# Kernel optimization log

Hardware: AMD Instinct MI355X
Metric: run time of the kernel (lower is better)

Reference implementation:

```python
import jax, jax.numpy as jnp
import numpy as np

EPS = 1e-6
AREA_WIDTH = 3
NHEAD = 8
DIM = 16


def _skew(v):
    # v: [N,3] -> [N,3,3] cross-product matrix
    x, y, z = v[..., 0], v[..., 1], v[..., 2]
    zero = jnp.zeros_like(x)
    return jnp.stack([
        jnp.stack([zero, -z, y], -1),
        jnp.stack([z, zero, -x], -1),
        jnp.stack([-y, x, zero], -1)], -2)


def _create_meshgrid(h, w):
    # kornia create_meshgrid(..., normalized=False): last dim is (x, y), row-major flatten
    xs = jnp.arange(w, dtype=jnp.float32)
    ys = jnp.arange(h, dtype=jnp.float32)
    gx, gy = jnp.meshgrid(xs, ys, indexing='xy')  # [h,w]
    return jnp.stack([gx, gy], -1).reshape(h * w, 2)  # [S,2]


def _epipolar_lines(coord, R, t, K0, K1):
    # coord [S,2]; R [N,3,3]; t [N,3,1] -> lines [N,S,3] (unit-normalized a,b), mode [N,S]
    S = coord.shape[0]
    p = jnp.concatenate([coord, jnp.ones((S, 1), coord.dtype)], -1)  # [S,3]
    E = _skew(t[..., 0]) @ R                                         # [t]_x R
    F = jnp.swapaxes(jnp.linalg.inv(K1), -1, -2) @ E @ jnp.linalg.inv(K0)
    lines = jnp.einsum('nij,sj->nsi', F, p)
    n = jnp.linalg.norm(lines[..., :2], axis=-1, keepdims=True)
    lines = lines / jnp.maximum(n, 1e-12)
    mode = jnp.abs(lines[..., 1]) >= jnp.abs(lines[..., 0])  # True: solve y(x) (|b|>=|a|)
    return lines, mode


def _get_mask(lines, mode, coord, area_width):
    # lines [N,L,3], mode [N,L], coord [S,2] -> within [N,L,S]
    a, b, c = lines[..., 0], lines[..., 1], lines[..., 2]
    xs, ys = coord[:, 0], coord[:, 1]
    hw = area_width / 2.0
    safe = lambda d: jnp.where(jnp.abs(d) < 1e-12, 1e-12, d)
    cy = (-a / safe(b))[..., None] * xs + (-c / safe(b))[..., None]  # [N,L,S]
    cx = (-b / safe(a))[..., None] * ys + (-c / safe(a))[..., None]
    wy = (ys < cy + hw) & (ys > cy - hw)
    wx = (xs < cx + hw) & (xs > cx - hw)
    return jnp.where(mode[..., None], wy, wx)


def _gather_index(within, C):
    # sort-based top-C compaction, index 0 doubles as padding (faithful to source)
    S = within.shape[-1]
    idx = jnp.arange(S, dtype=jnp.int32)
    ti = jnp.where(within, idx[None, None, :], 0)
    ti = jnp.sort(ti, axis=-1)[..., -C:]
    return ti, ti != 0


def _feature_map(x):
    return jax.nn.elu(x) + 1.0


def reference(queries, keys, values, solved_sample, K0, K1, R, t, h0c, w0c, scale):
    N, L, H, D = queries.shape
    sol = np.asarray(solved_sample).astype(bool)  # static split of the batch
    sol_idx = np.nonzero(sol)[0]
    uns_idx = np.nonzero(~sol)[0]
    Q = _feature_map(queries)
    K = _feature_map(keys)
    out = jnp.zeros((N, L, H, D), queries.dtype)

    if sol_idx.size > 0:  # epipolar-gathered candidate attention, direction '0to1'
        coord = _create_meshgrid(h0c, w0c)
        K0s = K0[sol_idx].at[:, :2, :].mul(1.0 / scale)
        K1s = K1[sol_idx].at[:, :2, :].mul(1.0 / scale)
        C = max(h0c, w0c) * AREA_WIDTH
        lines, mode = _epipolar_lines(coord, R[sol_idx], t[sol_idx], K0s, K1s)
        within = _get_mask(lines, mode, coord, AREA_WIDTH)       # [Ns,L,S]
        index, mask = _gather_index(within, C)                    # [Ns,L,C]
        Ns = sol_idx.size
        n_ix = jnp.arange(Ns)[:, None, None]
        Qs = Q[sol_idx]
        Ks = K[sol_idx][n_ix, index]            # [Ns,L,C,H,D]
        Vs = values[sol_idx][n_ix, index]
        m = mask[..., None, None].astype(Ks.dtype)
        Ks = Ks * m
        Vs = Vs * m / C
        KV = jnp.einsum('nlchd,nlchv->nlhdv', Ks, Vs)
        Z = 1.0 / (jnp.einsum('nlhd,nlhd->nlh', Qs, Ks.sum(2)) + EPS)
        out = out.at[sol_idx].set(jnp.einsum('nlhd,nlhdv,nlh->nlhv', Qs, KV, Z) * C)

    if uns_idx.size > 0:  # plain linear attention
        Qu, Ku, Vu = Q[uns_idx], K[uns_idx], values[uns_idx]
        S = Ku.shape[1]
        KV = jnp.einsum('nshd,nshv->nhdv', Ku, Vu / S)
        Z = 1.0 / (jnp.einsum('nlhd,nhd->nlh', Qu, Ku.sum(1)) + EPS)
        out = out.at[uns_idx].set(jnp.einsum('nlhd,nhdv,nlh->nlhv', Qu, KV, Z) * S)
    return out


def setup_inputs() -> dict:
    key = jax.random.key(0)
    kq, kk, kv = jax.random.split(key, 3)
    N, H, D = 4, NHEAD, DIM
    h0c, w0c = 48, 64
    L = h0c * w0c
    queries = jax.random.normal(kq, (N, L, H, D), jnp.float32)
    keys = jax.random.normal(kk, (N, L, H, D), jnp.float32)
    values = jax.random.normal(kv, (N, L, H, D), jnp.float32)
    solved_sample = jnp.array([True, True, False, False])
    Kmat = np.array([[600., 0., 256.], [0., 600., 192.], [0., 0., 1.]], np.float32)
    K0 = jnp.asarray(np.tile(Kmat, (N, 1, 1)))
    Rl, tl = [], []
    for i in range(N):
        th = 0.05 * (i + 1)
        Rl.append(np.array([[np.cos(th), 0., np.sin(th)], [0., 1., 0.],
                            [-np.sin(th), 0., np.cos(th)]], np.float32))
        tl.append(np.array([[0.2 + 0.01 * i], [0.05], [0.02]], np.float32))
    R = jnp.asarray(np.stack(Rl))
    t = jnp.asarray(np.stack(tl))
    return {"queries": queries, "keys": keys, "values": values,
            "solved_sample": solved_sample, "K0": K0, "K1": K0, "R": R, "t": t,
            "h0c": h0c, "w0c": w0c, "scale": 8}
```

## Files before the change

### kernel.cpp

```cpp
#include <hip/hip_runtime.h>
#include <math.h>

#define NHEAD 8
#define DIM   16
#define EPSF  1e-6f
#define KVCH  8

typedef _Float16 half2_t __attribute__((ext_vector_type(2)));
typedef _Float16 half4_t __attribute__((ext_vector_type(4)));
typedef _Float16 half8_t __attribute__((ext_vector_type(8)));

#if defined(__has_builtin)
#if __has_builtin(__builtin_amdgcn_fdot2)
#define HAVE_FDOT2 1
#endif
#endif

__device__ __forceinline__ float dot2(half2_t a, half2_t b, float c) {
#ifdef HAVE_FDOT2
    return __builtin_amdgcn_fdot2(a, b, c, false);
#else
    return c + (float)a.x * (float)b.x + (float)a.y * (float)b.y;
#endif
}

__device__ __forceinline__ bool solved_flag(const void* p, int i) {
    const unsigned int* u = (const unsigned int*)p;
    unsigned int v0 = u[0];
    if (v0 <= 1u)             return u[i] != 0u;
    if (v0 == 0x3F800000u)    return ((const float*)p)[i] != 0.0f;
    return ((const unsigned char*)p)[i] != 0;
}

__device__ __forceinline__ float fm(float x) {
    return x > 0.f ? x + 1.f : expf(x);
}

__device__ void inv3d(const double* M, double* inv) {
    double det = M[0]*(M[4]*M[8]-M[5]*M[7]) - M[1]*(M[3]*M[8]-M[5]*M[6]) + M[2]*(M[3]*M[7]-M[4]*M[6]);
    double id = 1.0 / det;
    inv[0] =  (M[4]*M[8]-M[5]*M[7])*id;
    inv[1] = -(M[1]*M[8]-M[2]*M[7])*id;
    inv[2] =  (M[1]*M[5]-M[2]*M[4])*id;
    inv[3] = -(M[3]*M[8]-M[5]*M[6])*id;
    inv[4] =  (M[0]*M[8]-M[2]*M[6])*id;
    inv[5] = -(M[0]*M[5]-M[2]*M[3])*id;
    inv[6] =  (M[3]*M[7]-M[4]*M[6])*id;
    inv[7] = -(M[0]*M[7]-M[1]*M[6])*id;
    inv[8] =  (M[0]*M[4]-M[1]*M[3])*id;
}

__device__ void compute_F_one(const float* K0, const float* K1, const float* R,
                              const float* t, float invs, float* Fout, int n) {
    double A[9], B[9];
    for (int i = 0; i < 9; ++i) {
        float a = K0[n*9 + i], b = K1[n*9 + i];
        if (i < 6) { a *= invs; b *= invs; }
        A[i] = (double)a; B[i] = (double)b;
    }
    double iA[9], iB[9];
    inv3d(A, iA); inv3d(B, iB);
    double tx = t[n*3+0], ty = t[n*3+1], tz = t[n*3+2];
    double S[9] = {0.0,-tz,ty, tz,0.0,-tx, -ty,tx,0.0};
    double E[9], M[9];
    for (int i = 0; i < 3; ++i)
        for (int j = 0; j < 3; ++j) {
            double s = 0.0;
            for (int k = 0; k < 3; ++k) s += S[i*3+k] * (double)R[n*9 + k*3 + j];
            E[i*3+j] = s;
        }
    for (int i = 0; i < 3; ++i)
        for (int j = 0; j < 3; ++j) {
            double s = 0.0;
            for (int k = 0; k < 3; ++k) s += E[i*3+k] * iA[k*3+j];
            M[i*3+j] = s;
        }
    for (int i = 0; i < 3; ++i)
        for (int j = 0; j < 3; ++j) {
            double s = 0.0;
            for (int k = 0; k < 3; ++k) s += iB[k*3+i] * M[k*3+j];
            Fout[n*9 + i*3 + j] = (float)s;
        }
}

__launch_bounds__(256)
__global__ void prep_kv(const float4* __restrict__ Kr4, const float4* __restrict__ Vr4,
                        _Float16* __restrict__ Kh, _Float16* __restrict__ Vh, int n4,
                        const float* __restrict__ Kr, const float* __restrict__ Vr,
                        const void* __restrict__ flags,
                        float* __restrict__ KVp, float* __restrict__ Ksp,
                        const float* __restrict__ K0, const float* __restrict__ K1,
                        const float* __restrict__ R,  const float* __restrict__ t,
                        const int* __restrict__ scale_p, float* __restrict__ Fout,
                        int N, int L, int PB) {
    if ((int)blockIdx.x < PB) {
        int i = blockIdx.x * 256 + threadIdx.x;
        if (i < n4) {
            float4 k = Kr4[i];
            half4_t kh = { (_Float16)fm(k.x), (_Float16)fm(k.y), (_Float16)fm(k.z), (_Float16)fm(k.w) };
            ((half4_t*)Kh)[i] = kh;
            float4 v = Vr4[i];
            half4_t vh = { (_Float16)v.x, (_Float16)v.y, (_Float16)v.z, (_Float16)v.w };
            ((half4_t*)Vh)[i] = vh;
        }
        if (blockIdx.x == 0) {
            if (threadIdx.x < (unsigned)N) {
                float invs = 1.0f / (float)(*scale_p);
                compute_F_one(K0, K1, R, t, invs, Fout, threadIdx.x);
            }
            if (threadIdx.x >= 64 && threadIdx.x < 192) {
                int tz = threadIdx.x - 64;
                size_t zr = (size_t)N * L * 128 + tz;
                Kh[zr] = (_Float16)0.f;
                Vh[zr] = (_Float16)0.f;
            }
        }
    } else {
        int kb = blockIdx.x - PB;
        int chunk = kb & (KVCH - 1);
        int h = (kb >> 3) & 7;
        int n = kb >> 6;
        if (n >= N || solved_flag(flags, n)) return;
        int tdx = threadIdx.x;
        int d = tdx >> 4, v = tdx & 15;
        int rowsPer = (L + KVCH - 1) / KVCH;
        int r0 = chunk * rowsPer;
        int r1 = min(r0 + rowsPer, L);
        const float* Kb = Kr + (size_t)n * L * (NHEAD * DIM) + h * DIM;
        const float* Vb = Vr + (size_t)n * L * (NHEAD * DIM) + h * DIM;
        float acc = 0.f, ks = 0.f;
        #pragma unroll 8
        for (int s = r0; s < r1; ++s) {
            float kd = fm(Kb[(size_t)s * (NHEAD * DIM) + d]);
            float vv = Vb[(size_t)s * (NHEAD * DIM) + v];
            acc += kd * vv;
            ks  += kd;
        }
        KVp[(((size_t)chunk * N + n) * NHEAD + h) * 256 + (d << 4) + v] = acc;
        if (v == 0) Ksp[(((size_t)chunk * N + n) * NHEAD + h) * 16 + d] = ks;
    }
}

__launch_bounds__(256)
__global__ void mega(const float* __restrict__ Qr,
                     const _Float16* __restrict__ Kh, const _Float16* __restrict__ Vh,
                     const void* __restrict__ flags,  const float* __restrict__ F,
                     const float* __restrict__ KVp,   const float* __restrict__ Ksp,
                     float* __restrict__ outp,
                     const int* __restrict__ h0c_p, const int* __restrict__ w0c_p,
                     int N, int L, int Bs) {
    __shared__ int    tbl[4][96];
    __shared__ float2 comb[2][64];
    __shared__ float  dcomb[2][8];
    if ((int)blockIdx.x < Bs) {
        int w    = threadIdx.x >> 6;
        int p    = w & 1;
        int qp   = w >> 1;
        int lane = threadIdx.x & 63;
        int q    = blockIdx.x * 2 + qp;
        int n    = q / L;
        if (n >= N) return;
        if (!solved_flag(flags, n)) return;
        int NL = N * L;
        int s = q - n * L;
        int W  = *w0c_p;
        int Hc = *h0c_p;
        float px = (float)(s % W);
        float py = (float)(s / W);

        const float* Fn = F + n * 9;
        float a = Fn[0]*px + Fn[1]*py + Fn[2];
        float b = Fn[3]*px + Fn[4]*py + Fn[5];
        float c = Fn[6]*px + Fn[7]*py + Fn[8];
        float nrm = sqrtf(a*a + b*b);
        float mdiv = fmaxf(nrm, 1e-12f);
        a /= mdiv; b /= mdiv; c /= mdiv;
        bool mode = fabsf(b) >= fabsf(a);

        float slope, inter;
        int outerN, innerMax, sI, sO;
        if (mode) {
            float bs = (fabsf(b) < 1e-12f) ? 1e-12f : b;
            slope = -a / bs; inter = -c / bs;
            outerN = W; innerMax = Hc; sI = W; sO = 1;
        } else {
            float as = (fabsf(a) < 1e-12f) ? 1e-12f : a;
            slope = -b / as; inter = -c / as;
            outerN = Hc; innerMax = W; sI = 1; sO = W;
        }

        int c8 = lane >> 3;
        int h  = lane & 7;
        int h16 = h << 4;

        const float4* q4 = (const float4*)(Qr + (size_t)q * (NHEAD * DIM) + h16);
        half2_t q2[8];
        {
            float4 a0 = q4[0], a1 = q4[1], a2 = q4[2], a3 = q4[3];
            q2[0] = (half2_t){ (_Float16)fm(a0.x), (_Float16)fm(a0.y) };
            q2[1] = (half2_t){ (_Float16)fm(a0.z), (_Float16)fm(a0.w) };
            q2[2] = (half2_t){ (_Float16)fm(a1.x), (_Float16)fm(a1.y) };
            q2[3] = (half2_t){ (_Float16)fm(a1.z), (_Float16)fm(a1.w) };
            q2[4] = (half2_t){ (_Float16)fm(a2.x), (_Float16)fm(a2.y) };
            q2[5] = (half2_t){ (_Float16)fm(a2.z), (_Float16)fm(a2.w) };
            q2[6] = (half2_t){ (_Float16)fm(a3.x), (_Float16)fm(a3.y) };
            q2[7] = (half2_t){ (_Float16)fm(a3.z), (_Float16)fm(a3.w) };
        }

        int totalC = outerN * 3;
        int zsent  = NL << 7;
        const float hw = 1.5f;
        for (int tt = lane; tt < 96; tt += 64) {
            int g = tt >> 3, c8t = tt & 7;
            int m = (g << 4) | (p << 3) | c8t;
            int o = (int)((unsigned)m / 3u);
            int j = m - o * 3;
            float cc = fmaf(slope, (float)o, inter);
            float lo = cc - hw, hi = cc + hw;
            int ii = (int)floorf(lo) + 1 + j;
            float fi = (float)ii;
            bool valid = (m < totalC) && (ii >= 0) && (ii < innerMax)
                         && (fi > lo) && (fi < hi);
            int s2 = ii * sI + o * sO;
            valid = valid && (s2 != 0);
            tbl[w][tt] = valid ? ((n * L + s2) << 7) : zsent;
        }
        __syncthreads();

        half2_t acc2[8];
        #pragma unroll
        for (int i = 0; i < 8; ++i) acc2[i] = (half2_t){ (_Float16)0.f, (_Float16)0.f };
        float den = 0.f;

        int groups = (totalC + 15) >> 4;
        #pragma unroll 3
        for (int g = 0; g < groups; ++g) {
            int entry = tbl[w][(g << 3) + c8];
            const half8_t* kr = (const half8_t*)(Kh + entry + h16);
            const half8_t* vr = (const half8_t*)(Vh + entry + h16);
            half8_t k0 = kr[0], k1 = kr[1];
            half8_t v0 = vr[0], v1 = vr[1];
            union H8 { half8_t v; half2_t h[4]; };
            H8 ku0, ku1, vu0, vu1;
            ku0.v = k0; ku1.v = k1; vu0.v = v0; vu1.v = v1;
            float sA = 0.f, sB = 0.f;
            sA = dot2(q2[0], ku0.h[0], sA);
            sB = dot2(q2[1], ku0.h[1], sB);
            sA = dot2(q2[2], ku0.h[2], sA);
            sB = dot2(q2[3], ku0.h[3], sB);
            sA = dot2(q2[4], ku1.h[0], sA);
            sB = dot2(q2[5], ku1.h[1], sB);
            sA = dot2(q2[6], ku1.h[2], sA);
            sB = dot2(q2[7], ku1.h[3], sB);
            float sc = sA + sB;
            den += sc;
            _Float16 sch = (_Float16)sc;
            half2_t scv = (half2_t){ sch, sch };
            acc2[0] += scv * vu0.h[0];
            acc2[1] += scv * vu0.h[1];
            acc2[2] += scv * vu0.h[2];
            acc2[3] += scv * vu0.h[3];
            acc2[4] += scv * vu1.h[0];
            acc2[5] += scv * vu1.h[1];
            acc2[6] += scv * vu1.h[2];
            acc2[7] += scv * vu1.h[3];
        }

        den += __shfl_xor(den, 8);
        den += __shfl_xor(den, 16);
        den += __shfl_xor(den, 32);

        bool hi8 = (lane & 8) != 0;
        half2_t t4[4];
        #pragma unroll
        for (int j2 = 0; j2 < 4; ++j2) {
            half2_t send = hi8 ? acc2[j2] : acc2[4 + j2];
            int rr = __shfl_xor(__builtin_bit_cast(int, send), 8);
            half2_t keep = hi8 ? acc2[4 + j2] : acc2[j2];
            t4[j2] = keep + __builtin_bit_cast(half2_t, rr);
        }
        bool hi16 = (lane & 16) != 0;
        half2_t t2[2];
        #pragma unroll
        for (int j2 = 0; j2 < 2; ++j2) {
            half2_t send = hi16 ? t4[j2] : t4[2 + j2];
            int rr = __shfl_xor(__builtin_bit_cast(int, send), 16);
            half2_t keep = hi16 ? t4[2 + j2] : t4[j2];
            t2[j2] = keep + __builtin_bit_cast(half2_t, rr);
        }
        bool hi32 = (lane & 32) != 0;
        half2_t t1;
        {
            half2_t send = hi32 ? t2[0] : t2[1];
            int rr = __shfl_xor(__builtin_bit_cast(int, send), 32);
            half2_t keep = hi32 ? t2[1] : t2[0];
            t1 = keep + __builtin_bit_cast(half2_t, rr);
        }
        int e0 = (hi8 ? 8 : 0) + (hi16 ? 4 : 0) + (hi32 ? 2 : 0);

        if (p == 1) {
            comb[qp][lane] = make_float2((float)t1.x, (float)t1.y);
            if (lane < 8) dcomb[qp][lane] = den;
        }
        __syncthreads();
        if (p == 0) {
            float2 oth = comb[qp][lane];
            float dtot = den + dcomb[qp][h];
            float r = 1.0f / (dtot + EPSF);
            float2 o2 = { ((float)t1.x + oth.x) * r, ((float)t1.y + oth.y) * r };
            *(float2*)(outp + (size_t)q * (NHEAD * DIM) + h16 + e0) = o2;
        }
    } else {
        long long tot2 = (long long)N * L * NHEAD * DIM / 2;
        long long idx2 = (long long)(blockIdx.x - Bs) * 256 + threadIdx.x;
        if (idx2 >= tot2) return;
        int pp = (int)(idx2 & 63);
        int h = pp >> 3;
        int v = (pp & 7) * 2;
        long long ns = idx2 >> 6;
        int n = (int)(ns / L);
        if (solved_flag(flags, n)) return;
        const float* qrow = Qr + ns * (NHEAD * DIM) + h * DIM;
        float num0 = 0.f, num1 = 0.f, den = 0.f;
        #pragma unroll
        for (int d = 0; d < 16; ++d) {
            float qd = fm(qrow[d]);
            #pragma unroll
            for (int cch = 0; cch < KVCH; ++cch) {
                const float2 kv2 = *(const float2*)(KVp + (((size_t)cch * N + n) * NHEAD + h) * 256 + (d << 4) + v);
                num0 += qd * kv2.x;
                num1 += qd * kv2.y;
                den  += qd * Ksp[(((size_t)cch * N + n) * NHEAD + h) * 16 + d];
            }
        }
        float rdiv = 1.0f / (den + EPSF);
        size_t ob = ns * (NHEAD * DIM) + h * DIM + v;
        outp[ob]     = num0 * rdiv;
        outp[ob + 1] = num1 * rdiv;
    }
}

extern "C" void kernel_launch(void* const* d_in, const int* in_sizes, int n_in,
                              void* d_out, int out_size, void* d_ws, size_t ws_size,
                              hipStream_t stream) {
    const float* Qr   = (const float*)d_in[0];
    const float* Kr   = (const float*)d_in[1];
    const float* Vr   = (const float*)d_in[2];
    const void*  flag = d_in[3];
    const float* K0   = (const float*)d_in[4];
    const float* K1   = (const float*)d_in[5];
    const float* R    = (const float*)d_in[6];
    const float* t    = (const float*)d_in[7];
    const int*   h0c  = (const int*)d_in[8];
    const int*   w0c  = (const int*)d_in[9];
    const int*   scl  = (const int*)d_in[10];

    int N = in_sizes[3];
    int T = in_sizes[0];
    int L = T / (N * NHEAD * DIM);

    size_t arr = (size_t)T + 8 * 128;
    _Float16* Kh = (_Float16*)d_ws;
    _Float16* Vh = Kh + arr;
    float* Fm   = (float*)(Vh + arr);
    float* KVp  = Fm + (size_t)N * 9;
    float* Ksp  = KVp + (size_t)KVCH * N * NHEAD * 256;

    float* outp = (float*)d_out;

    int n4 = T / 4;
    int PB = (n4 + 255) / 256;
    int KB = N * NHEAD * KVCH;
    prep_kv<<<PB + KB, 256, 0, stream>>>((const float4*)Kr, (const float4*)Vr,
                                         Kh, Vh, n4, Kr, Vr, flag, KVp, Ksp,
                                         K0, K1, R, t, scl, Fm, N, L, PB);

    int Bs = (N * L) / 2;
    long long tot2 = (long long)N * L * NHEAD * DIM / 2;
    int Bu = (int)((tot2 + 255) / 256);
    mega<<<Bs + Bu, 256, 0, stream>>>(Qr, Kh, Vh, flag, Fm, KVp, Ksp, outp,
                                      h0c, w0c, N, L, Bs);
}
```

Baseline: 178.5 us.

## Process one query per wavefront with split-head lane mapping

Each wavefront now handles one full query instead of two wavefronts splitting a query's candidates. Lanes pair up to cover the 16-dim heads in halves, and dot products are combined with a lane-1 shuffle. This removes the cross-wavefront shared-memory combine and its second barrier, and halves the number of blocks. The cost is more shuffle reductions over all accumulators, plus an output store done by only 16 lanes. The index-table offsets are rescaled to byte offsets.

```diff
diff --git a/kernel.cpp b/kernel.cpp
--- a/kernel.cpp
+++ b/kernel.cpp
@@ -149,15 +149,11 @@
                      float* __restrict__ outp,
                      const int* __restrict__ h0c_p, const int* __restrict__ w0c_p,
                      int N, int L, int Bs) {
-    __shared__ int    tbl[4][96];
-    __shared__ float2 comb[2][64];
-    __shared__ float  dcomb[2][8];
+    __shared__ int tbl[4][192];
     if ((int)blockIdx.x < Bs) {
         int w    = threadIdx.x >> 6;
-        int p    = w & 1;
-        int qp   = w >> 1;
         int lane = threadIdx.x & 63;
-        int q    = blockIdx.x * 2 + qp;
+        int q    = blockIdx.x * 4 + w;
         int n    = q / L;
         if (n >= N) return;
         if (!solved_flag(flags, n)) return;
@@ -191,28 +187,26 @@
 
         int c8 = lane >> 3;
         int h  = lane & 7;
-        int h16 = h << 4;
-
-        const float4* q4 = (const float4*)(Qr + (size_t)q * (NHEAD * DIM) + h16);
-        half2_t q2[8];
+
+        const float4* qb = (const float4*)(Qr + (size_t)q * (NHEAD * DIM));
+        half2_t ql[4], qh[4];
         {
-            float4 a0 = q4[0], a1 = q4[1], a2 = q4[2], a3 = q4[3];
-            q2[0] = (half2_t){ (_Float16)fm(a0.x), (_Float16)fm(a0.y) };
-            q2[1] = (half2_t){ (_Float16)fm(a0.z), (_Float16)fm(a0.w) };
-            q2[2] = (half2_t){ (_Float16)fm(a1.x), (_Float16)fm(a1.y) };
-            q2[3] = (half2_t){ (_Float16)fm(a1.z), (_Float16)fm(a1.w) };
-            q2[4] = (half2_t){ (_Float16)fm(a2.x), (_Float16)fm(a2.y) };
-            q2[5] = (half2_t){ (_Float16)fm(a2.z), (_Float16)fm(a2.w) };
-            q2[6] = (half2_t){ (_Float16)fm(a3.x), (_Float16)fm(a3.y) };
-            q2[7] = (half2_t){ (_Float16)fm(a3.z), (_Float16)fm(a3.w) };
+            float4 a0 = qb[2*h], a1 = qb[2*h + 1];
+            float4 b0 = qb[16 + 2*h], b1 = qb[16 + 2*h + 1];
+            ql[0] = (half2_t){ (_Float16)fm(a0.x), (_Float16)fm(a0.y) };
+            ql[1] = (half2_t){ (_Float16)fm(a0.z), (_Float16)fm(a0.w) };
+            ql[2] = (half2_t){ (_Float16)fm(a1.x), (_Float16)fm(a1.y) };
+            ql[3] = (half2_t){ (_Float16)fm(a1.z), (_Float16)fm(a1.w) };
+            qh[0] = (half2_t){ (_Float16)fm(b0.x), (_Float16)fm(b0.y) };
+            qh[1] = (half2_t){ (_Float16)fm(b0.z), (_Float16)fm(b0.w) };
+            qh[2] = (half2_t){ (_Float16)fm(b1.x), (_Float16)fm(b1.y) };
+            qh[3] = (half2_t){ (_Float16)fm(b1.z), (_Float16)fm(b1.w) };
         }
 
         int totalC = outerN * 3;
-        int zsent  = NL << 7;
+        int zsent  = NL << 8;
         const float hw = 1.5f;
-        for (int tt = lane; tt < 96; tt += 64) {
-            int g = tt >> 3, c8t = tt & 7;
-            int m = (g << 4) | (p << 3) | c8t;
+        for (int m = lane; m < 192; m += 64) {
             int o = (int)((unsigned)m / 3u);
             int j = m - o * 3;
             float cc = fmaf(slope, (float)o, inter);
@@ -223,92 +217,81 @@
                          && (fi > lo) && (fi < hi);
             int s2 = ii * sI + o * sO;
             valid = valid && (s2 != 0);
-            tbl[w][tt] = valid ? ((n * L + s2) << 7) : zsent;
+            tbl[w][m] = valid ? ((n * L + s2) << 8) : zsent;
         }
         __syncthreads();
 
-        half2_t acc2[8];
+        half2_t accl[4], acch[4];
         #pragma unroll
-        for (int i = 0; i < 8; ++i) acc2[i] = (half2_t){ (_Float16)0.f, (_Float16)0.f };
-        float den = 0.f;
-
-        int groups = (totalC + 15) >> 4;
+        for (int i = 0; i < 4; ++i) {
+            accl[i] = (half2_t){ (_Float16)0.f, (_Float16)0.f };
+            acch[i] = (half2_t){ (_Float16)0.f, (_Float16)0.f };
+        }
+        float denl = 0.f, denh = 0.f;
+
+        int groups = (totalC + 7) >> 3;
+        int hoff = h << 4;
         #pragma unroll 3
         for (int g = 0; g < groups; ++g) {
-            int entry = tbl[w][(g << 3) + c8];
-            const half8_t* kr = (const half8_t*)(Kh + entry + h16);
-            const half8_t* vr = (const half8_t*)(Vh + entry + h16);
-            half8_t k0 = kr[0], k1 = kr[1];
-            half8_t v0 = vr[0], v1 = vr[1];
+            int off = tbl[w][(g << 3) + c8];
+            const char* kp = (const char*)Kh + off + hoff;
+            const char* vp = (const char*)Vh + off + hoff;
+            half8_t klo = *(const half8_t*)kp;
+            half8_t khi = *(const half8_t*)(kp + 128);
+            half8_t vlo = *(const half8_t*)vp;
+            half8_t vhi = *(const half8_t*)(vp + 128);
             union H8 { half8_t v; half2_t h[4]; };
-            H8 ku0, ku1, vu0, vu1;
-            ku0.v = k0; ku1.v = k1; vu0.v = v0; vu1.v = v1;
-            float sA = 0.f, sB = 0.f;
-            sA = dot2(q2[0], ku0.h[0], sA);
-            sB = dot2(q2[1], ku0.h[1], sB);
-            sA = dot2(q2[2], ku0.h[2], sA);
-            sB = dot2(q2[3], ku0.h[3], sB);
-            sA = dot2(q2[4], ku1.h[0], sA);
-            sB = dot2(q2[5], ku1.h[1], sB);
-            sA = dot2(q2[6], ku1.h[2], sA);
-            sB = dot2(q2[7], ku1.h[3], sB);
-            float sc = sA + sB;
-            den += sc;
-            _Float16 sch = (_Float16)sc;
-            half2_t scv = (half2_t){ sch, sch };
-            acc2[0] += scv * vu0.h[0];
-            acc2[1] += scv * vu0.h[1];
-            acc2[2] += scv * vu0.h[2];
-            acc2[3] += scv * vu0.h[3];
-            acc2[4] += scv * vu1.h[0];
-            acc2[5] += scv * vu1.h[1];
-            acc2[6] += scv * vu1.h[2];
-            acc2[7] += scv * vu1.h[3];
-        }
-
-        den += __shfl_xor(den, 8);
-        den += __shfl_xor(den, 16);
-        den += __shfl_xor(den, 32);
-
-        bool hi8 = (lane & 8) != 0;
-        half2_t t4[4];
+            H8 kl, kh2, vl, vh2;
+            kl.v = klo; kh2.v = khi; vl.v = vlo; vh2.v = vhi;
+            float pl = 0.f, ph = 0.f;
+            pl = dot2(ql[0], kl.h[0], pl);
+            ph = dot2(qh[0], kh2.h[0], ph);
+            pl = dot2(ql[1], kl.h[1], pl);
+            ph = dot2(qh[1], kh2.h[1], ph);
+            pl = dot2(ql[2], kl.h[2], pl);
+            ph = dot2(qh[2], kh2.h[2], ph);
+            pl = dot2(ql[3], kl.h[3], pl);
+            ph = dot2(qh[3], kh2.h[3], ph);
+            float sl = pl + __shfl_xor(pl, 1);
+            float sh = ph + __shfl_xor(ph, 1);
+            denl += sl;
+            denh += sh;
+            _Float16 slh = (_Float16)sl, shh = (_Float16)sh;
+            half2_t slv = (half2_t){ slh, slh };
+            half2_t shv = (half2_t){ shh, shh };
+            accl[0] += slv * vl.h[0];  acch[0] += shv * vh2.h[0];
+            accl[1] += slv * vl.h[1];  acch[1] += shv * vh2.h[1];
+            accl[2] += slv * vl.h[2];  acch[2] += shv * vh2.h[2];
+            accl[3] += slv * vl.h[3];  acch[3] += shv * vh2.h[3];
+        }
+
         #pragma unroll
-        for (int j2 = 0; j2 < 4; ++j2) {
-            half2_t send = hi8 ? acc2[j2] : acc2[4 + j2];
-            int rr = __shfl_xor(__builtin_bit_cast(int, send), 8);
-            half2_t keep = hi8 ? acc2[4 + j2] : acc2[j2];
-            t4[j2] = keep + __builtin_bit_cast(half2_t, rr);
-        }
-        bool hi16 = (lane & 16) != 0;
-        half2_t t2[2];
-        #pragma unroll
-        for (int j2 = 0; j2 < 2; ++j2) {
-            half2_t send = hi16 ? t4[j2] : t4[2 + j2];
-            int rr = __shfl_xor(__builtin_bit_cast(int, send), 16);
-            half2_t keep = hi16 ? t4[2 + j2] : t4[j2];
-            t2[j2] = keep + __builtin_bit_cast(half2_t, rr);
-        }
-        bool hi32 = (lane & 32) != 0;
-        half2_t t1;
-        {
-            half2_t send = hi32 ? t2[0] : t2[1];
-            int rr = __shfl_xor(__builtin_bit_cast(int, send), 32);
-            half2_t keep = hi32 ? t2[1] : t2[0];
-            t1 = keep + __builtin_bit_cast(half2_t, rr);
-        }
-        int e0 = (hi8 ? 8 : 0) + (hi16 ? 4 : 0) + (hi32 ? 2 : 0);
-
-        if (p == 1) {
-            comb[qp][lane] = make_float2((float)t1.x, (float)t1.y);
-            if (lane < 8) dcomb[qp][lane] = den;
-        }
-        __syncthreads();
-        if (p == 0) {
-            float2 oth = comb[qp][lane];
-            float dtot = den + dcomb[qp][h];
-            float r = 1.0f / (dtot + EPSF);
-            float2 o2 = { ((float)t1.x + oth.x) * r, ((float)t1.y + oth.y) * r };
-            *(float2*)(outp + (size_t)q * (NHEAD * DIM) + h16 + e0) = o2;
+        for (int off2 = 8; off2 < 64; off2 <<= 1) {
+            denl += __shfl_xor(denl, off2);
+            denh += __shfl_xor(denh, off2);
+            #pragma unroll
+            for (int i = 0; i < 4; ++i) {
+                int rl = __shfl_xor(__builtin_bit_cast(int, accl[i]), off2);
+                int rh = __shfl_xor(__builtin_bit_cast(int, acch[i]), off2);
+                accl[i] += __builtin_bit_cast(half2_t, rl);
+                acch[i] += __builtin_bit_cast(half2_t, rh);
+            }
+        }
+
+        if (lane < 16) {
+            int hh = lane & 7;
+            bool hi = lane >= 8;
+            half2_t a0 = hi ? acch[0] : accl[0];
+            half2_t a1 = hi ? acch[1] : accl[1];
+            half2_t a2 = hi ? acch[2] : accl[2];
+            half2_t a3 = hi ? acch[3] : accl[3];
+            float den = hi ? denh : denl;
+            float r = 1.0f / (den + EPSF);
+            float* op = outp + (size_t)q * (NHEAD * DIM) + (hi ? 64 : 0) + 8 * hh;
+            float4 o0 = { (float)a0.x * r, (float)a0.y * r, (float)a1.x * r, (float)a1.y * r };
+            float4 o1 = { (float)a2.x * r, (float)a2.y * r, (float)a3.x * r, (float)a3.y * r };
+            *(float4*)op       = o0;
+            *(float4*)(op + 4) = o1;
         }
     } else {
         long long tot2 = (long long)N * L * NHEAD * DIM / 2;
@@ -375,7 +358,7 @@
                                          Kh, Vh, n4, Kr, Vr, flag, KVp, Ksp,
                                          K0, K1, R, t, scl, Fm, N, L, PB);
 
-    int Bs = (N * L) / 2;
+    int Bs = (N * L) / 4;
     long long tot2 = (long long)N * L * NHEAD * DIM / 2;
     int Bu = (int)((tot2 + 255) / 256);
     mega<<<Bs + Bu, 256, 0, stream>>>(Qr, Kh, Vh, flag, Fm, KVp, Ksp, outp,
```

Result: no change. 177.3 us (-0.7%).
